# Kernel tuning notes

Hardware: AMD Instinct MI355X
Metric: run time of the kernel (lower is better)

The kernel has to match this reference:

```python
import jax, jax.numpy as jnp
import numpy as np
import math

H = 12  # num_heads
LOGIT_SCALE_MAX = math.log(1.0 / 0.01)  # ~4.60517


def setup_inputs() -> dict:
    key = jax.random.key(0)
    ks = jax.random.split(key, 4)
    L, N, C = 1024, 8, 768
    scale = (C // H) ** -0.5
    return {
        "x": jax.random.normal(ks[0], (L, N, C), jnp.float32),
        "in_proj_weight": jax.random.normal(ks[1], (3 * C, C), jnp.float32) * scale,
        "in_proj_bias": jnp.zeros((3 * C,), jnp.float32),
        "logit_scale": jnp.full((H, 1, 1), jnp.log(10.0), jnp.float32),
        "head_scale": jnp.ones((H, 1, 1), jnp.float32),
        "out_w": jax.random.normal(ks[2], (C, C), jnp.float32) * scale,
        "out_b": jnp.zeros((C,), jnp.float32),
    }


def _normalize(t, eps=1e-12):
    # torch F.normalize: x / max(||x||, eps)
    n = jnp.linalg.norm(t, axis=-1, keepdims=True)
    return t / jnp.maximum(n, eps)


def reference(x, in_proj_weight, in_proj_bias, logit_scale, head_scale, out_w, out_b):
    L, N, C = x.shape
    D = C // H
    qkv = x @ in_proj_weight.T + in_proj_bias  # (L, N, 3C)
    q, k, v = jnp.split(qkv, 3, axis=-1)

    def to_heads(t):  # (L, N, C) -> (N, H, L, D); matches view(L, N*H, D).transpose(0,1)
        return t.reshape(L, N, H, D).transpose(1, 2, 0, 3)

    q, k, v = to_heads(q), to_heads(k), to_heads(v)
    # scaled-cosine attention: cosine sim * clamped-exp learnable logit scale
    attn = jnp.einsum('nhld,nhmd->nhlm', _normalize(q), _normalize(k))  # (N,H,L,L)
    ls = jnp.exp(jnp.minimum(logit_scale, LOGIT_SCALE_MAX))  # (H,1,1)
    attn = attn * ls[None]
    attn = jax.nn.softmax(attn, axis=-1)
    o = jnp.einsum('nhlm,nhmd->nhld', attn, v)  # (N,H,L,D)
    o = o * head_scale[None]  # per-head scale
    o = o.transpose(2, 0, 1, 3).reshape(L, N, C)  # back to (L, N, C)
    return o @ out_w.T + out_b
```

## Files before the change

kernel.cpp:

```cpp
#include <hip/hip_runtime.h>
#include <stdint.h>
#include <math.h>

typedef unsigned short u16;
typedef _Float16 f16;
typedef __attribute__((ext_vector_type(4))) float f32x4;
typedef __attribute__((ext_vector_type(8))) f16 h8;
typedef __attribute__((ext_vector_type(4))) f16 h4;
typedef __attribute__((ext_vector_type(2))) f16 h2;
typedef __attribute__((ext_vector_type(2))) __fp16 fp16x2;
typedef __attribute__((ext_vector_type(2))) unsigned int u32x2;
typedef __attribute__((ext_vector_type(4))) unsigned int u32x4;
typedef __attribute__((ext_vector_type(4))) unsigned short u16x4;
typedef __attribute__((ext_vector_type(8))) unsigned short u16x8;

typedef const __attribute__((address_space(1))) u16 gas_u16;
typedef __attribute__((address_space(3))) u16 las_u16;

#define MFMA32(a,b,c) __builtin_amdgcn_mfma_f32_16x16x32_f16((a),(b),(c),0,0,0)
#define MFMA16(a,b,c) __builtin_amdgcn_mfma_f32_16x16x16f16((a),(b),(c),0,0,0)

__device__ __forceinline__ float h2f(u16 h){ f16 x; __builtin_memcpy(&x,&h,2); return (float)x; }
__device__ __forceinline__ u16 f2h(float f){ f16 x = (f16)f; u16 u; __builtin_memcpy(&u,&x,2); return u; }

__device__ __forceinline__ float fast_exp2(float x){
#if __has_builtin(__builtin_amdgcn_exp2f)
  return __builtin_amdgcn_exp2f(x);
#else
  return exp2f(x);
#endif
}

__device__ __forceinline__ h2 pkrtz(float a, float b){
  fp16x2 t = __builtin_amdgcn_cvt_pkrtz(a, b);
  h2 r; __builtin_memcpy(&r, &t, 4);
  return r;
}

#define NA4 1572864
#define NB4 442368
#define NC4 147456
__global__ __launch_bounds__(256) void cvt3_kernel(
    const float* __restrict__ a, u16* __restrict__ da,
    const float* __restrict__ b, u16* __restrict__ db,
    const float* __restrict__ c, u16* __restrict__ dc)
{
  int i = blockIdx.x*256 + threadIdx.x;
  const float* s; u16* d; int off;
  if (i < NA4)            { s = a; d = da; off = i; }
  else if (i < NA4+NB4)   { s = b; d = db; off = i - NA4; }
  else if (i < NA4+NB4+NC4){ s = c; d = dc; off = i - NA4 - NB4; }
  else return;
  f32x4 v = ((const f32x4*)s)[off];
  u16x4 o;
  o[0]=f2h(v[0]); o[1]=f2h(v[1]); o[2]=f2h(v[2]); o[3]=f2h(v[3]);
  ((u16x4*)d)[off] = o;
}

#define GSLOT 24576
__global__ __launch_bounds__(512, 2) void gemm_kernel(
    const u16* __restrict__ A, const u16* __restrict__ B, const float* __restrict__ bias,
    int mode, u16* __restrict__ qh, u16* __restrict__ kh, u16* __restrict__ vtp,
    float* __restrict__ outp, const float* __restrict__ lsb)
{
  __shared__ u16 L[3*GSLOT];
  const int tid = threadIdx.x;
  const int lane = tid & 63;
  const int w = tid >> 6;
  const int wm = w >> 2, wn = w & 3;
  const int lo = lane & 15, hi = lane >> 4;

  const int bx = blockIdx.x, by = blockIdx.y;

  f32x4 zero = {0.f,0.f,0.f,0.f};
  f32x4 acc[4][4];
#pragma unroll
  for (int a=0;a<4;a++)
#pragma unroll
    for (int b=0;b<4;b++) acc[a][b] = zero;
  const u16* Ag = A + (size_t)bx*128*768;
  const u16* Bg = B + (size_t)by*256*768;
  const int srow = tid >> 3;
  const int scol = (((tid & 7) ^ (srow & 7)) * 8);

#define STG(slot, kt, half) do { \
    if ((half) == 0) { \
      __builtin_amdgcn_global_load_lds((gas_u16*)(Ag + (size_t)srow*768 + (kt) + scol),      (las_u16*)(&L[(slot)*GSLOT + tid*8]),        16, 0, 0); \
      __builtin_amdgcn_global_load_lds((gas_u16*)(Ag + (size_t)(srow+64)*768 + (kt) + scol), (las_u16*)(&L[(slot)*GSLOT + 4096 + tid*8]), 16, 0, 0); \
      __builtin_amdgcn_global_load_lds((gas_u16*)(Bg + (size_t)srow*768 + (kt) + scol),      (las_u16*)(&L[(slot)*GSLOT + 8192 + tid*8]), 16, 0, 0); \
    } else { \
      __builtin_amdgcn_global_load_lds((gas_u16*)(Bg + (size_t)(srow+64)*768 + (kt) + scol),  (las_u16*)(&L[(slot)*GSLOT + 12288 + tid*8]), 16, 0, 0); \
      __builtin_amdgcn_global_load_lds((gas_u16*)(Bg + (size_t)(srow+128)*768 + (kt) + scol), (las_u16*)(&L[(slot)*GSLOT + 16384 + tid*8]), 16, 0, 0); \
      __builtin_amdgcn_global_load_lds((gas_u16*)(Bg + (size_t)(srow+192)*768 + (kt) + scol), (las_u16*)(&L[(slot)*GSLOT + 20480 + tid*8]), 16, 0, 0); \
    } \
  } while(0)

  STG(0, 0, 0);  STG(0, 0, 1);
  STG(1, 64, 0); STG(1, 64, 1);
  asm volatile("s_waitcnt vmcnt(6)" ::: "memory");
  __builtin_amdgcn_sched_barrier(0);
  __builtin_amdgcn_s_barrier();

  int cs = 0;
  for (int t = 0; t < 12; ++t) {
    const u16* LA = L + cs*GSLOT;
    const u16* LB = LA + 8192;
    int ss = cs + 2; if (ss >= 3) ss -= 3;
#pragma unroll
    for (int kk = 0; kk < 2; ++kk) {
      const int rsl = ((hi + 4*kk) ^ (lo & 7)) * 8;
      h8 af[4], bfr[4];
#pragma unroll
      for (int mf=0; mf<4; mf++) af[mf]  = *(const h8*)(LA + (wm*64 + mf*16 + lo)*64 + rsl);
#pragma unroll
      for (int nf=0; nf<4; nf++) bfr[nf] = *(const h8*)(LB + (wn*64 + nf*16 + lo)*64 + rsl);
      if (t < 10) STG(ss, (t+2)*64, kk);
      __builtin_amdgcn_s_barrier();
      asm volatile("s_waitcnt lgkmcnt(0)" ::: "memory");
      __builtin_amdgcn_sched_barrier(0);
      __builtin_amdgcn_s_setprio(1);
#pragma unroll
      for (int mf=0; mf<4; mf++)
#pragma unroll
        for (int nf=0; nf<4; nf++)
          acc[mf][nf] = MFMA32(af[mf], bfr[nf], acc[mf][nf]);
      __builtin_amdgcn_s_setprio(0);
      if (kk == 1) {
        if (t < 10)       asm volatile("s_waitcnt vmcnt(6)" ::: "memory");
        else if (t == 10) asm volatile("s_waitcnt vmcnt(0)" ::: "memory");
        __builtin_amdgcn_sched_barrier(0);
      }
      __builtin_amdgcn_s_barrier();
    }
    cs += 1; if (cs >= 3) cs -= 3;
  }
#undef STG

  const int r0 = bx*128 + wm*64;
  const int j0 = by*256 + wn*64;
  if (mode == 0) {
    const int p = (j0 >= 1536) ? 2 : ((j0 >= 768) ? 1 : 0);
    float bi[4];
#pragma unroll
    for (int nf=0;nf<4;nf++) bi[nf] = bias[j0 + nf*16 + lo];
    if (p == 2) {
      u16* Tt = (u16*)L + wn*8192;
#pragma unroll
      for (int mf=0; mf<4; mf++)
#pragma unroll
        for (int nf=0; nf<4; nf++) {
          int d = nf*16 + lo;
          int c = wm*16 + mf*4 + hi;
          u16x4 pk;
#pragma unroll
          for (int i=0;i<4;i++) pk[i] = f2h(acc[mf][nf][i] + bi[nf]);
          *(u16x4*)(Tt + d*128 + ((c ^ ((d & 7) << 2)) << 2)) = pk;
        }
      __syncthreads();
#pragma unroll
      for (int kq=0; kq<8; kq++) {
        int idx = tid + kq*512;
        int nn  = idx & 7;
        int d   = (idx >> 3) & 63;
        int lh  = (idx >> 9) & 1;
        int tw  = idx >> 10;
        const u16* Ts = (const u16*)L + tw*8192;
        int hh = (by - 6)*4 + tw;
        u16x8 v8;
#pragma unroll
        for (int ll=0; ll<8; ll++) {
          int rl = (lh*8 + ll)*8 + nn;
          int c  = rl >> 2;
          v8[ll] = Ts[d*128 + ((c ^ ((d & 7) << 2)) << 2) + (rl & 3)];
        }
        size_t off = (((size_t)nn*12 + hh)*64 + d)*1024 + (size_t)bx*16 + lh*8;
        *(u16x8*)(vtp + off) = v8;
      }
    } else {
      const int c0 = j0 - p*768;
      const int hh = c0 >> 6;
      u16* dst = (p==0) ? qh : kh;
      float qsc = 1.0f;
      if (p == 0) qsc = __expf(fminf(lsb[hh], 4.6051701859880913680f)) * 1.4426950408889634f;
#pragma unroll
      for (int mf=0; mf<4; mf++)
#pragma unroll
        for (int i=0;i<4;i++) {
          int r = r0 + mf*16 + 4*hi + i;
          int n = r & 7, l = r >> 3;
          float v[4]; float ss2 = 0.f;
#pragma unroll
          for (int nf=0;nf<4;nf++){ v[nf] = acc[mf][nf][i] + bi[nf]; ss2 += v[nf]*v[nf]; }
          ss2 += __shfl_xor(ss2, 1);
          ss2 += __shfl_xor(ss2, 2);
          ss2 += __shfl_xor(ss2, 4);
          ss2 += __shfl_xor(ss2, 8);
          float sc = qsc / fmaxf(sqrtf(ss2), 1e-12f);
          size_t base = (((size_t)n*12 + hh)*1024 + l)*64;
#pragma unroll
          for (int nf=0;nf<4;nf++)
            dst[base + nf*16 + lo] = f2h(v[nf]*sc);
        }
    }
  } else {
#pragma unroll
    for (int nf=0; nf<4; nf++) {
      int j = j0 + nf*16 + lo;
      float bi = bias[j];
#pragma unroll
      for (int mf=0; mf<4; mf++)
#pragma unroll
        for (int i=0;i<4;i++) {
          int r = r0 + mf*16 + 4*hi + i;
          outp[(size_t)r*768 + j] = acc[mf][nf][i] + bi;
        }
    }
  }
}

__global__ __launch_bounds__(256, 3) void flash_kernel(
    const u16* __restrict__ qh, const u16* __restrict__ kh, const u16* __restrict__ vt,
    u16* __restrict__ obuf, const float* __restrict__ hsv, const float* __restrict__ lsp)
{
  __shared__ u16 lK[2][64*64];
  __shared__ u16 lVT[2][64*64];
  const int lin = blockIdx.y*8 + blockIdx.x;
  const int xcd = lin & 7, g = lin >> 3;
  const int nh = xcd + 8*(g >> 3);
  const int qt = g & 7;
  const int h = nh % 12, n = nh / 12;
  const u16* Qp = qh + (size_t)nh*65536;
  const u16* Kp = kh + (size_t)nh*65536;
  const u16* Vp = vt + (size_t)nh*65536;
  const int tid = threadIdx.x, lane = tid & 63, w = tid >> 6;
  const int lo = lane & 15, hi = lane >> 4;
  const int e = lo & 7;

  h8 qa0, qa1, qb0, qb1;
  {
    const u16* qrow = Qp + (size_t)(qt*128 + w*32 + lo)*64 + hi*8;
    qa0 = *(const h8*)qrow;          qa1 = *(const h8*)(qrow + 32);
    qb0 = *(const h8*)(qrow + 1024); qb1 = *(const h8*)(qrow + 1024 + 32);
  }
  const f32x4 zero = {0.f,0.f,0.f,0.f};
  f32x4 oA[4] = {zero,zero,zero,zero};
  f32x4 oB[4] = {zero,zero,zero,zero};
  f32x4 lA4 = zero, lB4 = zero;
  const h4 ones = {(f16)1.f,(f16)1.f,(f16)1.f,(f16)1.f};

  float OFF;
  {
    float b = __expf(fminf(lsp[h], 4.6051701859880913680f)) * 1.4426950408889634f;
    OFF = fmaxf(b - 15.5f, 0.f);
  }

  const int sr = tid >> 2;
  const int c4 = tid & 3;
  const int sx1 = sr & 7;
  const int sx2 = (sr & 7) << 1;

  u32x4 ka, kb, va, vb;
  ka = *(const u32x4*)(Kp + (size_t)sr*64 + c4*16);
  kb = *(const u32x4*)(Kp + (size_t)sr*64 + c4*16 + 8);
  va = *(const u32x4*)(Vp + (size_t)sr*1024 + c4*16);
  vb = *(const u32x4*)(Vp + (size_t)sr*1024 + c4*16 + 8);

#define STAGE_WRITE(bf) do { \
    u16* kr = lK[bf] + sr*64; \
    *(u32x4*)(kr + (((2*c4)   ^ sx1) << 3)) = ka; \
    *(u32x4*)(kr + (((2*c4+1) ^ sx1) << 3)) = kb; \
    u16* vr = lVT[bf] + sr*64; \
    *(u32x2*)(vr + (((( 0|c4) ^ sx2) << 2))) = (u32x2){va[0], va[1]}; \
    *(u32x2*)(vr + (((( 4|c4) ^ sx2) << 2))) = (u32x2){va[2], va[3]}; \
    *(u32x2*)(vr + (((( 8|c4) ^ sx2) << 2))) = (u32x2){vb[0], vb[1]}; \
    *(u32x2*)(vr + ((((12|c4) ^ sx2) << 2))) = (u32x2){vb[2], vb[3]}; \
  } while(0)

  STAGE_WRITE(0);
  asm volatile("s_waitcnt lgkmcnt(0)" ::: "memory");
  __builtin_amdgcn_sched_barrier(0);
  __builtin_amdgcn_s_barrier();

  for (int t = 0; t < 16; ++t) {
    const int cb = t & 1;
    if (t < 15) {
      ka = *(const u32x4*)(Kp + (size_t)(t+1)*4096 + (size_t)sr*64 + c4*16);
      kb = *(const u32x4*)(Kp + (size_t)(t+1)*4096 + (size_t)sr*64 + c4*16 + 8);
      va = *(const u32x4*)(Vp + (size_t)sr*1024 + (t+1)*64 + c4*16);
      vb = *(const u32x4*)(Vp + (size_t)sr*1024 + (t+1)*64 + c4*16 + 8);
    }
    f32x4 sa[4], sb[4];
#pragma unroll
    for (int kf=0; kf<4; kf++) {
      const u16* krow = lK[cb] + (kf*16 + lo)*64;
      h8 k0 = *(const h8*)(krow + (((hi  ) ^ e) << 3));
      h8 k1 = *(const h8*)(krow + (((hi+4) ^ e) << 3));
      sa[kf] = MFMA32(k1, qa1, MFMA32(k0, qa0, zero));
      sb[kf] = MFMA32(k1, qb1, MFMA32(k0, qb0, zero));
    }
    if (OFF != 0.f) {
#pragma unroll
      for (int kf=0;kf<4;kf++)
#pragma unroll
        for (int i=0;i<4;i++) { sa[kf][i] -= OFF; sb[kf][i] -= OFF; }
    }
    h4 pa[4], pb[4];
#pragma unroll
    for (int kf=0;kf<4;kf++) {
      h2 a01 = pkrtz(fast_exp2(sa[kf][0]), fast_exp2(sa[kf][1]));
      h2 a23 = pkrtz(fast_exp2(sa[kf][2]), fast_exp2(sa[kf][3]));
      pa[kf] = __builtin_shufflevector(a01, a23, 0, 1, 2, 3);
      h2 b01 = pkrtz(fast_exp2(sb[kf][0]), fast_exp2(sb[kf][1]));
      h2 b23 = pkrtz(fast_exp2(sb[kf][2]), fast_exp2(sb[kf][3]));
      pb[kf] = __builtin_shufflevector(b01, b23, 0, 1, 2, 3);
    }
#pragma unroll
    for (int kf=0;kf<4;kf++) {
      lA4 = MFMA16(ones, pa[kf], lA4);
      lB4 = MFMA16(ones, pb[kf], lB4);
    }
#pragma unroll
    for (int db=0; db<4; db++) {
      const u16* vrow = lVT[cb] + (db*16 + lo)*64;
      h8 v01 = *(const h8*)(vrow + ((((2*hi  ) ^ e) << 3)));
      h8 v23 = *(const h8*)(vrow + ((((2*hi+1) ^ e) << 3)));
      h4 f0 = __builtin_shufflevector(v01, v01, 0,1,2,3);
      h4 f1 = __builtin_shufflevector(v01, v01, 4,5,6,7);
      h4 f2 = __builtin_shufflevector(v23, v23, 0,1,2,3);
      h4 f3 = __builtin_shufflevector(v23, v23, 4,5,6,7);
      oA[db] = MFMA16(f0, pa[0], oA[db]);
      oB[db] = MFMA16(f0, pb[0], oB[db]);
      oA[db] = MFMA16(f1, pa[1], oA[db]);
      oB[db] = MFMA16(f1, pb[1], oB[db]);
      oA[db] = MFMA16(f2, pa[2], oA[db]);
      oB[db] = MFMA16(f2, pb[2], oB[db]);
      oA[db] = MFMA16(f3, pa[3], oA[db]);
      oB[db] = MFMA16(f3, pb[3], oB[db]);
    }
    if (t < 15) STAGE_WRITE(cb ^ 1);
    asm volatile("s_waitcnt lgkmcnt(0)" ::: "memory");
    __builtin_amdgcn_sched_barrier(0);
    __builtin_amdgcn_s_barrier();
  }
#undef STAGE_WRITE
  float hsc = hsv[h];
  float invA = hsc / lA4[0];
  float invB = hsc / lB4[0];
  int l0 = qt*128 + w*32 + lo;
  u16* dA = obuf + ((size_t)l0*8 + n)*768 + h*64;
  u16* dB = obuf + ((size_t)(l0+16)*8 + n)*768 + h*64;
#pragma unroll
  for (int db=0; db<4; db++) {
    u16x4 pk0, pk1;
#pragma unroll
    for (int i=0;i<4;i++) { pk0[i] = f2h(oA[db][i]*invA); pk1[i] = f2h(oB[db][i]*invB); }
    *(u16x4*)(dA + db*16 + hi*4) = pk0;
    *(u16x4*)(dB + db*16 + hi*4) = pk1;
  }
}

extern "C" void kernel_launch(void* const* d_in, const int* in_sizes, int n_in,
                              void* d_out, int out_size, void* d_ws, size_t ws_size,
                              hipStream_t stream)
{
  (void)in_sizes; (void)n_in; (void)out_size; (void)ws_size;
  const float* x  = (const float*)d_in[0];
  const float* w1 = (const float*)d_in[1];
  const float* b1 = (const float*)d_in[2];
  const float* ls = (const float*)d_in[3];
  const float* hs = (const float*)d_in[4];
  const float* w2 = (const float*)d_in[5];
  const float* b2 = (const float*)d_in[6];
  float* out = (float*)d_out;

  u16* x_bf  = (u16*)d_ws;
  u16* w1_bf = x_bf  + 6291456;
  u16* w2_bf = w1_bf + 1769472;
  u16* qh    = w2_bf + 589824;
  u16* kh    = qh    + 6291456;
  u16* vt    = kh    + 6291456;
  u16* ob    = x_bf;

  cvt3_kernel<<<8448, 256, 0, stream>>>(x, x_bf, w1, w1_bf, w2, w2_bf);
  gemm_kernel<<<dim3(64,9), 512, 0, stream>>>(x_bf, w1_bf, b1, 0, qh, kh, vt, nullptr, ls);
  flash_kernel<<<dim3(8,96), 256, 0, stream>>>(qh, kh, vt, ob, hs, ls);
  gemm_kernel<<<dim3(64,3), 512, 0, stream>>>(ob, w2_bf, b2, 1, nullptr, nullptr, nullptr, out, ls);
}
```

Baseline: 114.4 us.

## Load K and V fragments directly from global memory, dropping LDS staging

The flash attention kernel no longer stages K and V tiles through double-buffered shared memory with barriers. Each wave now loads its MFMA operand fragments straight from global memory (served by L1/L2) every iteration. This removes the LDS writes, the LDS reads and the per-tile workgroup barriers. In exchange, all four waves redundantly fetch the same K/V data and the loads are no longer prefetched one tile ahead, so more global traffic and exposed latency are possible.

```diff
diff --git a/kernel.cpp b/kernel.cpp
--- a/kernel.cpp
+++ b/kernel.cpp
@@ -222,8 +222,6 @@
     const u16* __restrict__ qh, const u16* __restrict__ kh, const u16* __restrict__ vt,
     u16* __restrict__ obuf, const float* __restrict__ hsv, const float* __restrict__ lsp)
 {
-  __shared__ u16 lK[2][64*64];
-  __shared__ u16 lVT[2][64*64];
   const int lin = blockIdx.y*8 + blockIdx.x;
   const int xcd = lin & 7, g = lin >> 3;
   const int nh = xcd + 8*(g >> 3);
@@ -234,7 +232,6 @@
   const u16* Vp = vt + (size_t)nh*65536;
   const int tid = threadIdx.x, lane = tid & 63, w = tid >> 6;
   const int lo = lane & 15, hi = lane >> 4;
-  const int e = lo & 7;
 
   h8 qa0, qa1, qb0, qb1;
   {
@@ -254,49 +251,28 @@
     OFF = fmaxf(b - 15.5f, 0.f);
   }
 
-  const int sr = tid >> 2;
-  const int c4 = tid & 3;
-  const int sx1 = sr & 7;
-  const int sx2 = (sr & 7) << 1;
-
-  u32x4 ka, kb, va, vb;
-  ka = *(const u32x4*)(Kp + (size_t)sr*64 + c4*16);
-  kb = *(const u32x4*)(Kp + (size_t)sr*64 + c4*16 + 8);
-  va = *(const u32x4*)(Vp + (size_t)sr*1024 + c4*16);
-  vb = *(const u32x4*)(Vp + (size_t)sr*1024 + c4*16 + 8);
-
-#define STAGE_WRITE(bf) do { \
-    u16* kr = lK[bf] + sr*64; \
-    *(u32x4*)(kr + (((2*c4)   ^ sx1) << 3)) = ka; \
-    *(u32x4*)(kr + (((2*c4+1) ^ sx1) << 3)) = kb; \
-    u16* vr = lVT[bf] + sr*64; \
-    *(u32x2*)(vr + (((( 0|c4) ^ sx2) << 2))) = (u32x2){va[0], va[1]}; \
-    *(u32x2*)(vr + (((( 4|c4) ^ sx2) << 2))) = (u32x2){va[2], va[3]}; \
-    *(u32x2*)(vr + (((( 8|c4) ^ sx2) << 2))) = (u32x2){vb[0], vb[1]}; \
-    *(u32x2*)(vr + ((((12|c4) ^ sx2) << 2))) = (u32x2){vb[2], vb[3]}; \
-  } while(0)
-
-  STAGE_WRITE(0);
-  asm volatile("s_waitcnt lgkmcnt(0)" ::: "memory");
-  __builtin_amdgcn_sched_barrier(0);
-  __builtin_amdgcn_s_barrier();
+  const u16* kbase = Kp + (size_t)lo*64 + hi*8;
+  const u16* vbase = Vp + (size_t)lo*1024 + hi*4;
 
   for (int t = 0; t < 16; ++t) {
-    const int cb = t & 1;
-    if (t < 15) {
-      ka = *(const u32x4*)(Kp + (size_t)(t+1)*4096 + (size_t)sr*64 + c4*16);
-      kb = *(const u32x4*)(Kp + (size_t)(t+1)*4096 + (size_t)sr*64 + c4*16 + 8);
-      va = *(const u32x4*)(Vp + (size_t)sr*1024 + (t+1)*64 + c4*16);
-      vb = *(const u32x4*)(Vp + (size_t)sr*1024 + (t+1)*64 + c4*16 + 8);
-    }
+    h8 k0[4], k1[4];
+#pragma unroll
+    for (int kf=0; kf<4; kf++) {
+      const u16* kr = kbase + (size_t)t*4096 + (size_t)kf*1024;
+      k0[kf] = *(const h8*)kr;
+      k1[kf] = *(const h8*)(kr + 32);
+    }
+    h4 vf[4][4];
+#pragma unroll
+    for (int db=0; db<4; db++)
+#pragma unroll
+      for (int kf=0; kf<4; kf++)
+        vf[db][kf] = *(const h4*)(vbase + (size_t)db*16384 + t*64 + kf*16);
     f32x4 sa[4], sb[4];
 #pragma unroll
     for (int kf=0; kf<4; kf++) {
-      const u16* krow = lK[cb] + (kf*16 + lo)*64;
-      h8 k0 = *(const h8*)(krow + (((hi  ) ^ e) << 3));
-      h8 k1 = *(const h8*)(krow + (((hi+4) ^ e) << 3));
-      sa[kf] = MFMA32(k1, qa1, MFMA32(k0, qa0, zero));
-      sb[kf] = MFMA32(k1, qb1, MFMA32(k0, qb0, zero));
+      sa[kf] = MFMA32(k1[kf], qa1, MFMA32(k0[kf], qa0, zero));
+      sb[kf] = MFMA32(k1[kf], qb1, MFMA32(k0[kf], qb0, zero));
     }
     if (OFF != 0.f) {
 #pragma unroll
@@ -321,28 +297,13 @@
     }
 #pragma unroll
     for (int db=0; db<4; db++) {
-      const u16* vrow = lVT[cb] + (db*16 + lo)*64;
-      h8 v01 = *(const h8*)(vrow + ((((2*hi  ) ^ e) << 3)));
-      h8 v23 = *(const h8*)(vrow + ((((2*hi+1) ^ e) << 3)));
-      h4 f0 = __builtin_shufflevector(v01, v01, 0,1,2,3);
-      h4 f1 = __builtin_shufflevector(v01, v01, 4,5,6,7);
-      h4 f2 = __builtin_shufflevector(v23, v23, 0,1,2,3);
-      h4 f3 = __builtin_shufflevector(v23, v23, 4,5,6,7);
-      oA[db] = MFMA16(f0, pa[0], oA[db]);
-      oB[db] = MFMA16(f0, pb[0], oB[db]);
-      oA[db] = MFMA16(f1, pa[1], oA[db]);
-      oB[db] = MFMA16(f1, pb[1], oB[db]);
-      oA[db] = MFMA16(f2, pa[2], oA[db]);
-      oB[db] = MFMA16(f2, pb[2], oB[db]);
-      oA[db] = MFMA16(f3, pa[3], oA[db]);
-      oB[db] = MFMA16(f3, pb[3], oB[db]);
-    }
-    if (t < 15) STAGE_WRITE(cb ^ 1);
-    asm volatile("s_waitcnt lgkmcnt(0)" ::: "memory");
-    __builtin_amdgcn_sched_barrier(0);
-    __builtin_amdgcn_s_barrier();
-  }
-#undef STAGE_WRITE
+#pragma unroll
+      for (int kf=0; kf<4; kf++) {
+        oA[db] = MFMA16(vf[db][kf], pa[kf], oA[db]);
+        oB[db] = MFMA16(vf[db][kf], pb[kf], oB[db]);
+      }
+    }
+  }
   float hsc = hsv[h];
   float invA = hsc / lA4[0];
   float invB = hsc / lB4[0];
```

Result: slower. 207.6 us (+81.5%).

## Software-pipeline attention loop: compute next tile's QK^T and exp before barrier-free PV

Applied to the files above, without the earlier changes.

Restructures the flash-attention inner loop so the QK^T and exp/pack of tile t+1 run right after the barrier, while the PV MFMAs of tile t run at the start of the next iteration. The global prefetch now runs two tiles ahead, and the LDS stage-write is issued before the PV work. The aim is to overlap the exp (VALU) stage with MFMA work and hide global/LDS latency. The cost is more live registers (the p fragments are held across iterations), which could reduce occupancy or cause spills.

```diff
diff --git a/kernel.cpp b/kernel.cpp
--- a/kernel.cpp
+++ b/kernel.cpp
@@ -260,10 +260,6 @@
   const int sx2 = (sr & 7) << 1;
 
   u32x4 ka, kb, va, vb;
-  ka = *(const u32x4*)(Kp + (size_t)sr*64 + c4*16);
-  kb = *(const u32x4*)(Kp + (size_t)sr*64 + c4*16 + 8);
-  va = *(const u32x4*)(Vp + (size_t)sr*1024 + c4*16);
-  vb = *(const u32x4*)(Vp + (size_t)sr*1024 + c4*16 + 8);
 
 #define STAGE_WRITE(bf) do { \
     u16* kr = lK[bf] + sr*64; \
@@ -276,44 +272,59 @@
     *(u32x2*)(vr + ((((12|c4) ^ sx2) << 2))) = (u32x2){vb[2], vb[3]}; \
   } while(0)
 
+#define PREFETCH(tt) do { \
+    ka = *(const u32x4*)(Kp + (size_t)(tt)*4096 + (size_t)sr*64 + c4*16); \
+    kb = *(const u32x4*)(Kp + (size_t)(tt)*4096 + (size_t)sr*64 + c4*16 + 8); \
+    va = *(const u32x4*)(Vp + (size_t)sr*1024 + (size_t)(tt)*64 + c4*16); \
+    vb = *(const u32x4*)(Vp + (size_t)sr*1024 + (size_t)(tt)*64 + c4*16 + 8); \
+  } while(0)
+
+#define QKT(dstA, dstB, buf) do { \
+    _Pragma("unroll") \
+    for (int kf=0; kf<4; kf++) { \
+      const u16* krow = lK[buf] + (kf*16 + lo)*64; \
+      h8 k0 = *(const h8*)(krow + (((hi  ) ^ e) << 3)); \
+      h8 k1 = *(const h8*)(krow + (((hi+4) ^ e) << 3)); \
+      dstA[kf] = MFMA32(k1, qa1, MFMA32(k0, qa0, zero)); \
+      dstB[kf] = MFMA32(k1, qb1, MFMA32(k0, qb0, zero)); \
+    } \
+  } while(0)
+
+#define EXPPACK() do { \
+    if (OFF != 0.f) { \
+      _Pragma("unroll") \
+      for (int kf=0;kf<4;kf++) \
+        _Pragma("unroll") \
+        for (int i=0;i<4;i++) { sa[kf][i] -= OFF; sb[kf][i] -= OFF; } \
+    } \
+    _Pragma("unroll") \
+    for (int kf=0;kf<4;kf++) { \
+      h2 a01 = pkrtz(fast_exp2(sa[kf][0]), fast_exp2(sa[kf][1])); \
+      h2 a23 = pkrtz(fast_exp2(sa[kf][2]), fast_exp2(sa[kf][3])); \
+      pa[kf] = __builtin_shufflevector(a01, a23, 0, 1, 2, 3); \
+      h2 b01 = pkrtz(fast_exp2(sb[kf][0]), fast_exp2(sb[kf][1])); \
+      h2 b23 = pkrtz(fast_exp2(sb[kf][2]), fast_exp2(sb[kf][3])); \
+      pb[kf] = __builtin_shufflevector(b01, b23, 0, 1, 2, 3); \
+    } \
+  } while(0)
+
+  h4 pa[4], pb[4];
+  PREFETCH(0);
   STAGE_WRITE(0);
   asm volatile("s_waitcnt lgkmcnt(0)" ::: "memory");
   __builtin_amdgcn_sched_barrier(0);
   __builtin_amdgcn_s_barrier();
+  PREFETCH(1);
+  {
+    f32x4 sa[4], sb[4];
+    QKT(sa, sb, 0);
+    EXPPACK();
+  }
 
   for (int t = 0; t < 16; ++t) {
-    const int cb = t & 1;
-    if (t < 15) {
-      ka = *(const u32x4*)(Kp + (size_t)(t+1)*4096 + (size_t)sr*64 + c4*16);
-      kb = *(const u32x4*)(Kp + (size_t)(t+1)*4096 + (size_t)sr*64 + c4*16 + 8);
-      va = *(const u32x4*)(Vp + (size_t)sr*1024 + (t+1)*64 + c4*16);
-      vb = *(const u32x4*)(Vp + (size_t)sr*1024 + (t+1)*64 + c4*16 + 8);
-    }
-    f32x4 sa[4], sb[4];
-#pragma unroll
-    for (int kf=0; kf<4; kf++) {
-      const u16* krow = lK[cb] + (kf*16 + lo)*64;
-      h8 k0 = *(const h8*)(krow + (((hi  ) ^ e) << 3));
-      h8 k1 = *(const h8*)(krow + (((hi+4) ^ e) << 3));
-      sa[kf] = MFMA32(k1, qa1, MFMA32(k0, qa0, zero));
-      sb[kf] = MFMA32(k1, qb1, MFMA32(k0, qb0, zero));
-    }
-    if (OFF != 0.f) {
-#pragma unroll
-      for (int kf=0;kf<4;kf++)
-#pragma unroll
-        for (int i=0;i<4;i++) { sa[kf][i] -= OFF; sb[kf][i] -= OFF; }
-    }
-    h4 pa[4], pb[4];
-#pragma unroll
-    for (int kf=0;kf<4;kf++) {
-      h2 a01 = pkrtz(fast_exp2(sa[kf][0]), fast_exp2(sa[kf][1]));
-      h2 a23 = pkrtz(fast_exp2(sa[kf][2]), fast_exp2(sa[kf][3]));
-      pa[kf] = __builtin_shufflevector(a01, a23, 0, 1, 2, 3);
-      h2 b01 = pkrtz(fast_exp2(sb[kf][0]), fast_exp2(sb[kf][1]));
-      h2 b23 = pkrtz(fast_exp2(sb[kf][2]), fast_exp2(sb[kf][3]));
-      pb[kf] = __builtin_shufflevector(b01, b23, 0, 1, 2, 3);
-    }
+    const int wb = (t+1) & 1;
+    const int vbuf = t & 1;
+    if (t < 15) STAGE_WRITE(wb);
 #pragma unroll
     for (int kf=0;kf<4;kf++) {
       lA4 = MFMA16(ones, pa[kf], lA4);
@@ -321,7 +332,7 @@
     }
 #pragma unroll
     for (int db=0; db<4; db++) {
-      const u16* vrow = lVT[cb] + (db*16 + lo)*64;
+      const u16* vrow = lVT[vbuf] + (db*16 + lo)*64;
       h8 v01 = *(const h8*)(vrow + ((((2*hi  ) ^ e) << 3)));
       h8 v23 = *(const h8*)(vrow + ((((2*hi+1) ^ e) << 3)));
       h4 f0 = __builtin_shufflevector(v01, v01, 0,1,2,3);
@@ -337,12 +348,20 @@
       oA[db] = MFMA16(f3, pa[3], oA[db]);
       oB[db] = MFMA16(f3, pb[3], oB[db]);
     }
-    if (t < 15) STAGE_WRITE(cb ^ 1);
-    asm volatile("s_waitcnt lgkmcnt(0)" ::: "memory");
-    __builtin_amdgcn_sched_barrier(0);
-    __builtin_amdgcn_s_barrier();
+    if (t < 15) {
+      asm volatile("s_waitcnt lgkmcnt(0)" ::: "memory");
+      __builtin_amdgcn_sched_barrier(0);
+      __builtin_amdgcn_s_barrier();
+      if (t < 14) PREFETCH(t+2);
+      f32x4 sa[4], sb[4];
+      QKT(sa, sb, wb);
+      EXPPACK();
+    }
   }
 #undef STAGE_WRITE
+#undef PREFETCH
+#undef QKT
+#undef EXPPACK
   float hsc = hsv[h];
   float invA = hsc / lA4[0];
   float invB = hsc / lB4[0];
```

Result: no change. 114.7 us, median of 2 (+0.2%).
